# Performance work log

Measured on AMD Instinct MI355X. Metric: run time of the kernel, lower is better.

## Reference

```python
import jax, jax.numpy as jnp
import numpy as np

HEADS, KV_HEADS, HEAD_DIM = 32, 8, 64


def apply_rope(x, cos, sin):
    # x: [b,h,s,d], cos/sin: [s, d//2]; pairs are interleaved (even/odd)
    c = cos[None, None, :, :]
    s = sin[None, None, :, :]
    x1 = x[..., 0::2]
    x2 = x[..., 1::2]
    xn = x1 * c - x2 * s
    yn = x1 * s + x2 * c
    return jnp.stack([xn, yn], axis=-1).reshape(x.shape)


def setup_inputs() -> dict:
    key = jax.random.key(0)
    ks = jax.random.split(key, 7)
    b, s, h = 1, 2048, 2048
    return {
        "x": jax.random.normal(ks[0], (b, s, h), jnp.float32),
        "cos": jax.random.normal(ks[1], (s, HEAD_DIM // 2), jnp.float32),
        "sin": jax.random.normal(ks[2], (s, HEAD_DIM // 2), jnp.float32),
        "Wq": jax.random.normal(ks[3], (h, HEADS * HEAD_DIM), jnp.float32) * 0.02,
        "Wk": jax.random.normal(ks[4], (h, KV_HEADS * HEAD_DIM), jnp.float32) * 0.02,
        "Wv": jax.random.normal(ks[5], (h, KV_HEADS * HEAD_DIM), jnp.float32) * 0.02,
        "Wo": jax.random.normal(ks[6], (HEADS * HEAD_DIM, h), jnp.float32) * 0.02,
    }


def reference(x, cos, sin, Wq, Wk, Wv, Wo):
    b, seq, hidden = x.shape
    Q = x @ Wq  # [b,s,H*d]
    K = x @ Wk  # [b,s,Kh*d]
    V = x @ Wv
    q = Q.reshape(b, seq, HEADS, HEAD_DIM).transpose(0, 2, 1, 3)      # b h s d
    k = K.reshape(b, seq, KV_HEADS, HEAD_DIM).transpose(0, 2, 1, 3)   # b k s d
    v = V.reshape(b, seq, KV_HEADS, HEAD_DIM).transpose(0, 2, 1, 3)
    r = HEADS // KV_HEADS
    # einops 'b k s d -> b (r k) s d': tile kv-head block r times
    k = jnp.tile(k, (1, r, 1, 1))
    v = jnp.tile(v, (1, r, 1, 1))
    q = apply_rope(q, cos, sin)
    k = apply_rope(k, cos, sin)
    scale = 1.0 / jnp.sqrt(jnp.float32(HEAD_DIM))
    qk = jnp.einsum('bhqd,bhkd->bhqk', q, k) * scale
    mask = jnp.triu(jnp.full((seq, seq), -jnp.inf, qk.dtype), k=1)
    attn = jax.nn.softmax(qk + mask, axis=-1)
    av = jnp.einsum('bhqk,bhkd->bhqd', attn, v)
    av = av.transpose(0, 2, 1, 3).reshape(b, seq, HEADS * HEAD_DIM)
    return av @ Wo
```

## Files before the change

### kernel.cpp

```cpp
#include <hip/hip_runtime.h>

typedef unsigned short u16;
typedef __attribute__((ext_vector_type(4))) float f32x4;
typedef __attribute__((ext_vector_type(16))) float f32x16;
typedef __attribute__((ext_vector_type(8))) __bf16 bf16x8;
typedef __attribute__((ext_vector_type(2))) __bf16 bf16x2;

#define HEADS 32
#define KV_HEADS 8
#define HD 64
#define SEQ 2048
#define HID 2048
#define NQK 3072
#define QSCALE (0.125f * 1.4426950408889634f)
#define OCH 2097152u

#define AS1 __attribute__((address_space(1)))
#define AS3 __attribute__((address_space(3)))

__device__ __forceinline__ u16 f2bf(float f) {
  unsigned u = __float_as_uint(f);
  u += 0x7FFFu + ((u >> 16) & 1u);
  return (u16)(u >> 16);
}

__device__ __forceinline__ unsigned pk2(float a, float b) {
  union { bf16x2 h; unsigned u; } c;
  c.h[0] = (__bf16)a; c.h[1] = (__bf16)b;
  return c.u;
}

__device__ __forceinline__ float bflo(unsigned u) {
  return __uint_as_float(u << 16);
}
__device__ __forceinline__ float bfhi(unsigned u) {
  return __uint_as_float(u & 0xFFFF0000u);
}

__device__ __forceinline__ void load16_to_lds(const void* g, void* l) {
  __builtin_amdgcn_global_load_lds((AS1 void*)(void*)g, (AS3 void*)l, 16, 0, 0);
}

__global__ __launch_bounds__(256) void k_prep(const float* __restrict__ x,
                                              const float* __restrict__ Wq,
                                              const float* __restrict__ Wk,
                                              const float* __restrict__ Wv,
                                              const float* __restrict__ Wo,
                                              u16* __restrict__ xb,
                                              u16* __restrict__ Wqkv,
                                              u16* __restrict__ WoT) {
  __shared__ float tile[32][33];
  int bid = blockIdx.x;
  if (bid < 4096) {
    int i = bid * 256 + threadIdx.x;
    float4 v = ((const float4*)x)[i];
    ushort4 o;
    o.x = f2bf(v.x); o.y = f2bf(v.y); o.z = f2bf(v.z); o.w = f2bf(v.w);
    ((ushort4*)xb)[i] = o;
    return;
  }
  const float* in; u16* out; int ldi, cx, cy;
  if (bid < 8192) {
    int b = bid - 4096;
    in = Wq; out = Wqkv; ldi = 2048; cx = b & 63; cy = b >> 6;
  } else if (bid < 9216) {
    int b = bid - 8192;
    in = Wk; out = Wqkv + (size_t)2048 * 2048; ldi = 512; cx = b & 15; cy = b >> 4;
  } else if (bid < 10240) {
    int b = bid - 9216;
    in = Wv; out = Wqkv + (size_t)2560 * 2048; ldi = 512; cx = b & 15; cy = b >> 4;
  } else {
    int b = bid - 10240;
    in = Wo; out = WoT; ldi = 2048; cx = b & 63; cy = b >> 6;
  }
  const int ldo = 2048;
  int c0 = cx * 32, r0 = cy * 32;
  int col = threadIdx.x & 31, rw = threadIdx.x >> 5;
#pragma unroll
  for (int i = 0; i < 4; i++)
    tile[rw + i * 8][col] = in[(size_t)(r0 + rw + i * 8) * ldi + c0 + col];
  __syncthreads();
#pragma unroll
  for (int i = 0; i < 4; i++)
    out[(size_t)(c0 + rw + i * 8) * ldo + r0 + col] = f2bf(tile[col][rw + i * 8]);
}

__device__ __forceinline__ void stage8(const u16* Ap, const u16* Bp, u16* AsX,
                                       u16* BsX, int tid, int K, int koff) {
#pragma unroll
  for (int i = 0; i < 4; i++) {
    load16_to_lds(Ap + (size_t)(i * 32) * K + koff, AsX + (i * 256 + tid) * 8);
    load16_to_lds(Bp + (size_t)(i * 32) * K + koff, BsX + (i * 256 + tid) * 8);
  }
}

__device__ __forceinline__ void frag16(const u16* Asb, const u16* Bsb,
                                       const int aoff[4][2], const int boff[4][2],
                                       f32x4 acc[4][4]) {
#pragma unroll
  for (int kk = 0; kk < 2; kk++) {
    bf16x8 a[4], b[4];
#pragma unroll
    for (int i = 0; i < 4; i++)
      a[i] = *(const bf16x8*)((const char*)Asb + aoff[i][kk]);
#pragma unroll
    for (int j = 0; j < 4; j++)
      b[j] = *(const bf16x8*)((const char*)Bsb + boff[j][kk]);
#pragma unroll
    for (int i = 0; i < 4; i++)
#pragma unroll
      for (int j = 0; j < 4; j++)
        acc[i][j] = __builtin_amdgcn_mfma_f32_16x16x32_bf16(a[i], b[j], acc[i][j], 0, 0, 0);
  }
}

#define TILE_STEP(AsX, BsX, tnext)                              \
  do {                                                          \
    asm volatile("s_waitcnt vmcnt(8)" ::: "memory");            \
    __builtin_amdgcn_sched_barrier(0);                          \
    __builtin_amdgcn_s_barrier();                               \
    frag16(AsX, BsX, aoff, boff, acc);                          \
    __builtin_amdgcn_sched_barrier(0);                          \
    __builtin_amdgcn_s_barrier();                               \
    stage8(Ap, Bp, AsX, BsX, tid, K, (tnext) * 64);             \
    __builtin_amdgcn_sched_barrier(0);                          \
  } while (0)

#define TILE_TAIL(AsX, BsX, n)                                  \
  do {                                                          \
    asm volatile("s_waitcnt vmcnt(" #n ")" ::: "memory");       \
    __builtin_amdgcn_sched_barrier(0);                          \
    __builtin_amdgcn_s_barrier();                               \
    frag16(AsX, BsX, aoff, boff, acc);                          \
  } while (0)

__global__ __launch_bounds__(256) void k_gemm(const u16* __restrict__ A,
                                              const u16* __restrict__ Bt,
                                              float* __restrict__ C,
                                              int M, int N, int K) {
  __shared__ u16 smem[32768];
  u16* As0 = smem;          u16* As1 = smem + 8192;
  u16* Bs0 = smem + 16384;  u16* Bs1 = smem + 24576;
  int tid = threadIdx.x;
  int m0 = blockIdx.x * 128, n0 = blockIdx.y * 128;
  int l = tid & 63, w = tid >> 6;
  int lr = l & 15, lg = l >> 4;
  int wr = (w >> 1) * 64, wc = (w & 1) * 64;
  f32x4 acc[4][4] = {};
  int r8 = tid >> 3;
  int sx = (tid & 7) ^ (r8 & 7);
  const u16* Ap = A + (size_t)(m0 + r8) * K + sx * 8;
  const u16* Bp = Bt + (size_t)(n0 + r8) * K + sx * 8;
  int aoff[4][2], boff[4][2];
#pragma unroll
  for (int i = 0; i < 4; i++) {
    int ra = wr + i * 16 + lr;
    int rb = wc + i * 16 + lr;
#pragma unroll
    for (int kk = 0; kk < 2; kk++) {
      aoff[i][kk] = ra * 128 + (((lg + kk * 4) ^ (ra & 7)) << 4);
      boff[i][kk] = rb * 128 + (((lg + kk * 4) ^ (rb & 7)) << 4);
    }
  }
  stage8(Ap, Bp, As0, Bs0, tid, K, 0);
  stage8(Ap, Bp, As1, Bs1, tid, K, 64);
#pragma unroll 1
  for (int t = 0; t < 30; t += 2) {
    TILE_STEP(As0, Bs0, t + 2);
    TILE_STEP(As1, Bs1, t + 3);
  }
  TILE_TAIL(As0, Bs0, 8);
  TILE_TAIL(As1, Bs1, 0);

#pragma unroll
  for (int i = 0; i < 4; i++)
#pragma unroll
    for (int j = 0; j < 4; j++)
#pragma unroll
      for (int r = 0; r < 4; r++)
        C[(size_t)(m0 + wr + i * 16 + lg * 4 + r) * N + n0 + wc + j * 16 + lr] =
            acc[i][j][r];
}

__device__ __forceinline__ void stageQ(const u16* Ap, const u16* Bp, u16* S,
                                       int tid, int koff) {
#pragma unroll
  for (int i = 0; i < 2; i++)
    load16_to_lds(Ap + (size_t)(i * 32) * HID + koff, S + (i * 256 + tid) * 8);
#pragma unroll
  for (int i = 0; i < 6; i++)
    load16_to_lds(Bp + (size_t)(i * 32) * HID + koff, S + 4096 + (i * 256 + tid) * 8);
}

__device__ __forceinline__ void frag26(const u16* Sb, const int aoff[2][2],
                                       const int boff[6][2], f32x4 acc[2][6]) {
#pragma unroll
  for (int kk = 0; kk < 2; kk++) {
    bf16x8 a[2], b[6];
#pragma unroll
    for (int i = 0; i < 2; i++)
      a[i] = *(const bf16x8*)((const char*)Sb + aoff[i][kk]);
#pragma unroll
    for (int j = 0; j < 6; j++)
      b[j] = *(const bf16x8*)((const char*)Sb + 8192 + boff[j][kk]);
    __builtin_amdgcn_s_setprio(1);
#pragma unroll
    for (int i = 0; i < 2; i++)
#pragma unroll
      for (int j = 0; j < 6; j++)
        acc[i][j] = __builtin_amdgcn_mfma_f32_16x16x32_bf16(a[i], b[j], acc[i][j], 0, 0, 0);
    __builtin_amdgcn_s_setprio(0);
  }
}

#define QK_STEP(Sc, tnext)                                      \
  do {                                                          \
    asm volatile("s_waitcnt vmcnt(8)" ::: "memory");            \
    __builtin_amdgcn_sched_barrier(0);                          \
    __builtin_amdgcn_s_barrier();                               \
    frag26(Sc, aoff, boff, acc);                                \
    __builtin_amdgcn_sched_barrier(0);                          \
    __builtin_amdgcn_s_barrier();                               \
    stageQ(Ap, Bp, Sc, tid, (tnext) * 64);                      \
    __builtin_amdgcn_sched_barrier(0);                          \
  } while (0)

#define QK_TAIL(Sc, n)                                          \
  do {                                                          \
    asm volatile("s_waitcnt vmcnt(" #n ")" ::: "memory");       \
    __builtin_amdgcn_sched_barrier(0);                          \
    __builtin_amdgcn_s_barrier();                               \
    frag26(Sc, aoff, boff, acc);                                \
  } while (0)

__global__ __launch_bounds__(256) void k_gemm_qkv(const u16* __restrict__ A,
                                                  const u16* __restrict__ Bt,
                                                  const float* __restrict__ cosp,
                                                  const float* __restrict__ sinp,
                                                  u16* __restrict__ qbuf,
                                                  u16* __restrict__ kbuf,
                                                  u16* __restrict__ vtb) {
  __shared__ u16 smem[32768];
  u16* S0 = smem;
  u16* S1 = smem + 16384;
  u16* Ts = smem;
  int tid = threadIdx.x;
  int bid = blockIdx.x;
  int wg = (bid & 7) * 64 + (bid >> 3);
  int m0 = (wg & 31) * 64, n0 = (wg >> 5) * 192;
  int l = tid & 63, w = tid >> 6;
  int lr = l & 15, lg = l >> 4;
  int wr = (w >> 1) * 32, wc = (w & 1) * 96;
  f32x4 acc[2][6] = {};
  int r8 = tid >> 3;
  int sx = (tid & 7) ^ (r8 & 7);
  const u16* Ap = A + (size_t)(m0 + r8) * HID + sx * 8;
  const u16* Bp = Bt + (size_t)(n0 + r8) * HID + sx * 8;
  int aoff[2][2], boff[6][2];
#pragma unroll
  for (int i = 0; i < 2; i++) {
    int ra = wr + i * 16 + lr;
#pragma unroll
    for (int kk = 0; kk < 2; kk++)
      aoff[i][kk] = ra * 128 + (((lg + kk * 4) ^ (ra & 7)) << 4);
  }
#pragma unroll
  for (int j = 0; j < 6; j++) {
    int rb = wc + j * 16 + lr;
#pragma unroll
    for (int kk = 0; kk < 2; kk++)
      boff[j][kk] = rb * 128 + (((lg + kk * 4) ^ (rb & 7)) << 4);
  }

  stageQ(Ap, Bp, S0, tid, 0);
  stageQ(Ap, Bp, S1, tid, 64);
#pragma unroll 1
  for (int t = 0; t < 30; t += 2) {
    QK_STEP(S0, t + 2);
    QK_STEP(S1, t + 3);
  }
  QK_TAIL(S0, 8);
  QK_TAIL(S1, 0);

  int odd = lr & 1;
#pragma unroll
  for (int j = 0; j < 6; j++) {
    int colf = n0 + wc + j * 16;
    if (colf < 2560) {
      bool isQ = colf < 2048;
      float scale = isQ ? QSCALE : 1.0f;
      u16* base = isQ ? qbuf + (size_t)(colf >> 6) * SEQ * HD
                      : kbuf + (size_t)((colf - 2048) >> 6) * SEQ * HD;
      int ch = colf & 63;
      int ii = (ch >> 1) + (lr >> 1);
#pragma unroll
      for (int i = 0; i < 2; i++)
#pragma unroll
        for (int r = 0; r < 4; r++) {
          float v = acc[i][j][r];
          float vp = __shfl_xor(v, 1, 64);
          int sr = m0 + wr + i * 16 + lg * 4 + r;
          float cs = cosp[sr * 32 + ii], sn = sinp[sr * 32 + ii];
          float x1 = odd ? vp : v, x2 = odd ? v : vp;
          float o = odd ? (x1 * sn + x2 * cs) : (x1 * cs - x2 * sn);
          base[(size_t)sr * HD + ch + lr] = f2bf(o * scale);
        }
    }
  }
  if (n0 + 192 > 2560) {
    __syncthreads();
#pragma unroll
    for (int j = 0; j < 6; j++) {
      int colf = n0 + wc + j * 16;
      if (colf >= 2560) {
#pragma unroll
        for (int i = 0; i < 2; i++)
#pragma unroll
          for (int r = 0; r < 4; r++) {
            int cB = wc + j * 16 + lr, rB = wr + i * 16 + lg * 4 + r;
            *(u16*)((char*)Ts + cB * 128 + ((rB * 2) ^ ((cB & 7) << 4))) =
                f2bf(acc[i][j][r]);
          }
      }
    }
    __syncthreads();
    int half = tid & 1;
#pragma unroll
    for (int p = 0; p < 2; p++) {
      int c = p * 128 + (tid >> 1);
      if (c < 192 && n0 + c >= 2560) {
        int col = n0 + c;
        int kvh = (col - 2560) >> 6, d = col & 63;
        u16* dst = vtb + (size_t)kvh * HD * SEQ + (size_t)d * SEQ + m0 + half * 32;
        const char* src = (const char*)Ts + c * 128;
        int cs7 = (c & 7) << 4;
#pragma unroll
        for (int q = 0; q < 4; q++)
          *(uint4*)(dst + q * 8) = *(const uint4*)(src + ((half * 64 + q * 16) ^ cs7));
      }
    }
  }
}

__global__ __launch_bounds__(256) void k_flash2(const u16* __restrict__ qb,
                                                const u16* __restrict__ kb,
                                                const u16* __restrict__ vt,
                                                unsigned* __restrict__ Opart,
                                                float2* __restrict__ ml) {
  __shared__ u16 Ks[2][64 * 64];
  __shared__ u16 Vs[2][64 * 64];
  int bid = blockIdx.x;
  int c = bid & 1;
  int b5 = bid >> 1;
  int h = b5 & 31;
  int qi = b5 >> 5;
  int qblk = (SEQ / 128) - 1 - qi;
  int kvh = h & 7;
  int tid = threadIdx.x, w = tid >> 6, l = tid & 63;
  int lq = l & 31, hi = l >> 5;
  const u16* qh = qb + (size_t)h * SEQ * HD;
  const u16* kh = kb + (size_t)kvh * SEQ * HD;
  const u16* vh = vt + (size_t)kvh * HD * SEQ;
  int wq0 = qblk * 128 + w * 32;
  int qg = wq0 + lq;

  bf16x8 qf[4];
#pragma unroll
  for (int ds = 0; ds < 4; ds++)
    qf[ds] = *(const bf16x8*)(qh + (size_t)qg * HD + ds * 16 + hi * 8);

  f32x16 acc[2] = {};
  float m_r = -__builtin_inff(), l_r = 0.f;

  int srow = tid >> 2, c4 = tid & 3, swz = (srow & 7) << 4;
  int sd0 = srow * 128 + ((c4 * 32) ^ swz);
  int sd1 = srow * 128 + ((c4 * 32 + 16) ^ swz);
  const int kt0 = c * (qblk + 1), kt1 = kt0 + qblk + 1;

  {
    const u16* ksrc = kh + (size_t)(kt0 * 64 + srow) * HD + c4 * 16;
    const u16* vsrc = vh + (size_t)srow * SEQ + kt0 * 64 + c4 * 16;
    uint4 a0 = *(const uint4*)(ksrc), a1 = *(const uint4*)(ksrc + 8);
    uint4 b0 = *(const uint4*)(vsrc), b1 = *(const uint4*)(vsrc + 8);
    *(uint4*)((char*)Ks[0] + sd0) = a0; *(uint4*)((char*)Ks[0] + sd1) = a1;
    *(uint4*)((char*)Vs[0] + sd0) = b0; *(uint4*)((char*)Vs[0] + sd1) = b1;
  }
  __syncthreads();

  uint4 kr0, kr1, vr0, vr1;
  int lswz = (lq & 7) << 4;
  for (int kt = kt0; kt < kt1; kt++) {
    int b = (kt - kt0) & 1;
    if (kt + 1 < kt1) {
      const u16* ksrc = kh + (size_t)((kt + 1) * 64 + srow) * HD + c4 * 16;
      const u16* vsrc = vh + (size_t)srow * SEQ + (kt + 1) * 64 + c4 * 16;
      kr0 = *(const uint4*)(ksrc); kr1 = *(const uint4*)(ksrc + 8);
      vr0 = *(const uint4*)(vsrc); vr1 = *(const uint4*)(vsrc + 8);
    }

    if (kt * 64 <= wq0 + 31) {
      f32x16 sT[2] = {};
      const char* kbase = (const char*)Ks[b];
      __builtin_amdgcn_s_setprio(1);
#pragma unroll
      for (int t = 0; t < 2; t++) {
#pragma unroll
        for (int ds = 0; ds < 4; ds++) {
          bf16x8 kf = *(const bf16x8*)(kbase + (t * 32 + lq) * 128 +
                                       ((ds * 32 + hi * 16) ^ lswz));
          sT[t] = __builtin_amdgcn_mfma_f32_32x32x16_bf16(kf, qf[ds], sT[t], 0, 0, 0);
        }
      }
      __builtin_amdgcn_s_setprio(0);

      if (kt * 64 + 63 > wq0) {
#pragma unroll
        for (int t = 0; t < 2; t++)
#pragma unroll
          for (int r = 0; r < 16; r++) {
            int kg = kt * 64 + t * 32 + (r & 3) + 8 * (r >> 2) + 4 * hi;
            if (kg > qg) sT[t][r] = -__builtin_inff();
          }
      }

      float pmax = sT[0][0];
#pragma unroll
      for (int r = 1; r < 16; r++) pmax = fmaxf(pmax, sT[0][r]);
#pragma unroll
      for (int r = 0; r < 16; r++) pmax = fmaxf(pmax, sT[1][r]);
      pmax = fmaxf(pmax, __shfl_xor(pmax, 32, 64));

      if (!__all(pmax <= m_r + 8.f)) {
        float mn = fmaxf(m_r, pmax);
        float scl = __builtin_amdgcn_exp2f(m_r - mn);
        l_r *= scl;
        acc[0] *= scl;
        acc[1] *= scl;
        m_r = mn;
      }

      float ss = 0.f;
#pragma unroll
      for (int t = 0; t < 2; t++)
#pragma unroll
        for (int r = 0; r < 16; r++) {
          float p = __builtin_amdgcn_exp2f(sT[t][r] - m_r);
          sT[t][r] = p;
          ss += p;
        }
      ss += __shfl_xor(ss, 32, 64);
      l_r += ss;

      const char* vbase = (const char*)Vs[b];
#pragma unroll
      for (int t = 0; t < 2; t++) {
        unsigned cp[4][2];
#pragma unroll
        for (int m = 0; m < 4; m++) {
          cp[m][0] = pk2(sT[t][4 * m + 0], sT[t][4 * m + 1]);
          cp[m][1] = pk2(sT[t][4 * m + 2], sT[t][4 * m + 3]);
        }
#pragma unroll
        for (int kl = 0; kl < 2; kl++) {
          unsigned s0 = hi ? cp[2 * kl][0] : cp[2 * kl + 1][0];
          unsigned s1 = hi ? cp[2 * kl][1] : cp[2 * kl + 1][1];
          unsigned r0 = (unsigned)__shfl_xor((int)s0, 32, 64);
          unsigned r1 = (unsigned)__shfl_xor((int)s1, 32, 64);
          union { unsigned u[4]; bf16x8 v; } pa;
          pa.u[0] = hi ? r0 : cp[2 * kl][0];
          pa.u[1] = hi ? r1 : cp[2 * kl][1];
          pa.u[2] = hi ? cp[2 * kl + 1][0] : r0;
          pa.u[3] = hi ? cp[2 * kl + 1][1] : r1;
          int ks = t * 2 + kl;
          __builtin_amdgcn_s_setprio(1);
#pragma unroll
          for (int dt = 0; dt < 2; dt++) {
            bf16x8 vb = *(const bf16x8*)(vbase + (dt * 32 + lq) * 128 +
                                         ((ks * 32 + hi * 16) ^ lswz));
            acc[dt] = __builtin_amdgcn_mfma_f32_32x32x16_bf16(vb, pa.v, acc[dt], 0, 0, 0);
          }
          __builtin_amdgcn_s_setprio(0);
        }
      }
    }

    if (kt + 1 < kt1) {
      *(uint4*)((char*)Ks[b ^ 1] + sd0) = kr0;
      *(uint4*)((char*)Ks[b ^ 1] + sd1) = kr1;
      *(uint4*)((char*)Vs[b ^ 1] + sd0) = vr0;
      *(uint4*)((char*)Vs[b ^ 1] + sd1) = vr1;
    }
    __syncthreads();
  }

  unsigned* op = Opart + (size_t)c * OCH + ((size_t)(b5 * 4 + w) * 16) * 64;
#pragma unroll
  for (int dt = 0; dt < 2; dt++)
#pragma unroll
    for (int j = 0; j < 8; j++)
      op[(dt * 8 + j) * 64 + l] = pk2(acc[dt][2 * j], acc[dt][2 * j + 1]);
  if (!hi)
    ml[c * (HEADS * SEQ) + h * SEQ + wq0 + lq] = make_float2(m_r, l_r);
}

__global__ __launch_bounds__(256) void k_merge(const unsigned* __restrict__ Opart,
                                               const float2* __restrict__ ml,
                                               u16* __restrict__ av) {
  __shared__ u16 Ts[8192];
  int bid = blockIdx.x;
  int h = bid & 31, qblk = bid >> 5;
  int b5 = ((SEQ / 128 - 1 - qblk) << 5) | h;
  int tid = threadIdx.x, w = tid >> 6, l = tid & 63;
  int lq = l & 31, hi = l >> 5;
  int wq0 = qblk * 128 + w * 32;

  float2 ml0 = ml[h * SEQ + wq0 + lq];
  float2 ml1 = ml[HEADS * SEQ + h * SEQ + wq0 + lq];
  float m = fmaxf(ml0.x, ml1.x);
  float f0 = __builtin_amdgcn_exp2f(ml0.x - m);
  float f1 = __builtin_amdgcn_exp2f(ml1.x - m);
  float inv = 1.0f / (ml0.y * f0 + ml1.y * f1);

  const unsigned* op0 = Opart + ((size_t)(b5 * 4 + w) * 16) * 64;
  const unsigned* op1 = op0 + OCH;
  f32x16 acc[2];
#pragma unroll
  for (int dt = 0; dt < 2; dt++)
#pragma unroll
    for (int j = 0; j < 8; j++) {
      unsigned a0 = op0[(dt * 8 + j) * 64 + l];
      unsigned a1 = op1[(dt * 8 + j) * 64 + l];
      acc[dt][2 * j] = bflo(a0) * f0 + bflo(a1) * f1;
      acc[dt][2 * j + 1] = bfhi(a0) * f0 + bfhi(a1) * f1;
    }

  int lswz = (lq & 7) << 4;
  char* wbase = (char*)Ts + w * 4096;
#pragma unroll
  for (int dt = 0; dt < 2; dt++)
#pragma unroll
    for (int m4 = 0; m4 < 4; m4++) {
      int r0 = 4 * m4;
      uint2 pr;
      pr.x = pk2(acc[dt][r0 + 0] * inv, acc[dt][r0 + 1] * inv);
      pr.y = pk2(acc[dt][r0 + 2] * inv, acc[dt][r0 + 3] * inv);
      int byte = lq * 128 + ((dt * 64 + m4 * 16 + hi * 8) ^ lswz);
      *(uint2*)(wbase + byte) = pr;
    }
  __syncthreads();
  int q2 = l >> 1, cH = l & 1;
  int qswz = (q2 & 7) << 4;
#pragma unroll
  for (int i = 0; i < 4; i++) {
    uint4 d = *(const uint4*)(wbase + q2 * 128 + ((cH * 64 + i * 16) ^ qswz));
    *(uint4*)(av + (size_t)(wq0 + q2) * HID + h * HD + cH * 32 + i * 8) = d;
  }
}

extern "C" void kernel_launch(void* const* d_in, const int* in_sizes, int n_in,
                              void* d_out, int out_size, void* d_ws, size_t ws_size,
                              hipStream_t stream) {
  (void)in_sizes; (void)n_in; (void)out_size; (void)ws_size;
  const float* x = (const float*)d_in[0];
  const float* cosp = (const float*)d_in[1];
  const float* sinp = (const float*)d_in[2];
  const float* Wq = (const float*)d_in[3];
  const float* Wk = (const float*)d_in[4];
  const float* Wv = (const float*)d_in[5];
  const float* Wo = (const float*)d_in[6];
  float* out = (float*)d_out;
  char* ws = (char*)d_ws;

  u16* xb = (u16*)(ws);
  float2* mlb = (float2*)(ws);
  u16* Wqkv = (u16*)(ws + ((size_t)8 << 20));
  u16* WoT = (u16*)(ws + ((size_t)20 << 20));
  u16* qbuf = (u16*)(ws + ((size_t)28 << 20));
  u16* kbuf = (u16*)(ws + ((size_t)36 << 20));
  u16* vtb = (u16*)(ws + ((size_t)38 << 20));
  u16* av = (u16*)(ws + ((size_t)40 << 20));
  unsigned* Opart = (unsigned*)(ws + ((size_t)48 << 20));

  k_prep<<<14336, 256, 0, stream>>>(x, Wq, Wk, Wv, Wo, xb, Wqkv, WoT);
  k_gemm_qkv<<<512, 256, 0, stream>>>(xb, Wqkv, cosp, sinp, qbuf, kbuf, vtb);
  k_flash2<<<(SEQ / 128) * HEADS * 2, 256, 0, stream>>>(qbuf, kbuf, vtb, Opart, mlb);
  k_merge<<<(SEQ / 128) * HEADS, 256, 0, stream>>>(Opart, mlb, av);
  k_gemm<<<dim3(SEQ / 128, HID / 128), 256, 0, stream>>>(av, WoT, out, SEQ, HID, HID);
}
```

Measured before the change: 116.0 us.

## Fuse split-KV merge into flash kernel via last-arriver atomic counter

Removes the separate k_merge launch. Each flash block fences its partial output, then bumps a per-(qblock,head) counter with an agent-scope atomic, and the second block to arrive does the merge and writes av. The counters live in the output buffer, are zeroed by block 0 of the QKV GEMM, and are later overwritten by the final GEMM. This saves one kernel launch and its tail, at the cost of an atomic and an imbalanced epilogue on the last-arriving blocks. It reuses Ks smem as scratch, which assumes the loop's final __syncthreads has completed.

```diff
diff --git a/kernel.cpp b/kernel.cpp
--- a/kernel.cpp
+++ b/kernel.cpp
@@ -239,12 +239,17 @@
                                                   const float* __restrict__ sinp,
                                                   u16* __restrict__ qbuf,
                                                   u16* __restrict__ kbuf,
-                                                  u16* __restrict__ vtb) {
+                                                  u16* __restrict__ vtb,
+                                                  unsigned* __restrict__ flags) {
   __shared__ u16 smem[32768];
   u16* S0 = smem;
   u16* S1 = smem + 16384;
   u16* Ts = smem;
   int tid = threadIdx.x;
+  if (blockIdx.x == 0) {
+    flags[tid] = 0;
+    flags[tid + 256] = 0;
+  }
   int bid = blockIdx.x;
   int wg = (bid & 7) * 64 + (bid >> 3);
   int m0 = (wg & 31) * 64, n0 = (wg >> 5) * 192;
@@ -346,9 +351,12 @@
                                                 const u16* __restrict__ kb,
                                                 const u16* __restrict__ vt,
                                                 unsigned* __restrict__ Opart,
-                                                float2* __restrict__ ml) {
+                                                float2* __restrict__ ml,
+                                                u16* __restrict__ av,
+                                                unsigned* __restrict__ flags) {
   __shared__ u16 Ks[2][64 * 64];
   __shared__ u16 Vs[2][64 * 64];
+  __shared__ unsigned winner;
   int bid = blockIdx.x;
   int c = bid & 1;
   int b5 = bid >> 1;
@@ -501,59 +509,54 @@
       op[(dt * 8 + j) * 64 + l] = pk2(acc[dt][2 * j], acc[dt][2 * j + 1]);
   if (!hi)
     ml[c * (HEADS * SEQ) + h * SEQ + wq0 + lq] = make_float2(m_r, l_r);
-}
-
-__global__ __launch_bounds__(256) void k_merge(const unsigned* __restrict__ Opart,
-                                               const float2* __restrict__ ml,
-                                               u16* __restrict__ av) {
-  __shared__ u16 Ts[8192];
-  int bid = blockIdx.x;
-  int h = bid & 31, qblk = bid >> 5;
-  int b5 = ((SEQ / 128 - 1 - qblk) << 5) | h;
-  int tid = threadIdx.x, w = tid >> 6, l = tid & 63;
-  int lq = l & 31, hi = l >> 5;
-  int wq0 = qblk * 128 + w * 32;
-
-  float2 ml0 = ml[h * SEQ + wq0 + lq];
-  float2 ml1 = ml[HEADS * SEQ + h * SEQ + wq0 + lq];
-  float m = fmaxf(ml0.x, ml1.x);
-  float f0 = __builtin_amdgcn_exp2f(ml0.x - m);
-  float f1 = __builtin_amdgcn_exp2f(ml1.x - m);
-  float inv = 1.0f / (ml0.y * f0 + ml1.y * f1);
-
-  const unsigned* op0 = Opart + ((size_t)(b5 * 4 + w) * 16) * 64;
-  const unsigned* op1 = op0 + OCH;
-  f32x16 acc[2];
-#pragma unroll
-  for (int dt = 0; dt < 2; dt++)
-#pragma unroll
-    for (int j = 0; j < 8; j++) {
-      unsigned a0 = op0[(dt * 8 + j) * 64 + l];
-      unsigned a1 = op1[(dt * 8 + j) * 64 + l];
-      acc[dt][2 * j] = bflo(a0) * f0 + bflo(a1) * f1;
-      acc[dt][2 * j + 1] = bfhi(a0) * f0 + bfhi(a1) * f1;
-    }
-
-  int lswz = (lq & 7) << 4;
-  char* wbase = (char*)Ts + w * 4096;
-#pragma unroll
-  for (int dt = 0; dt < 2; dt++)
-#pragma unroll
-    for (int m4 = 0; m4 < 4; m4++) {
-      int r0 = 4 * m4;
-      uint2 pr;
-      pr.x = pk2(acc[dt][r0 + 0] * inv, acc[dt][r0 + 1] * inv);
-      pr.y = pk2(acc[dt][r0 + 2] * inv, acc[dt][r0 + 3] * inv);
-      int byte = lq * 128 + ((dt * 64 + m4 * 16 + hi * 8) ^ lswz);
-      *(uint2*)(wbase + byte) = pr;
-    }
+
+  __threadfence();
   __syncthreads();
-  int q2 = l >> 1, cH = l & 1;
-  int qswz = (q2 & 7) << 4;
-#pragma unroll
-  for (int i = 0; i < 4; i++) {
-    uint4 d = *(const uint4*)(wbase + q2 * 128 + ((cH * 64 + i * 16) ^ qswz));
-    *(uint4*)(av + (size_t)(wq0 + q2) * HID + h * HD + cH * 32 + i * 8) = d;
+  if (tid == 0)
+    winner = __hip_atomic_fetch_add(&flags[b5], 1u, __ATOMIC_ACQ_REL,
+                                    __HIP_MEMORY_SCOPE_AGENT);
+  __syncthreads();
+  if (winner == 1) {
+    float2 ml0 = ml[h * SEQ + wq0 + lq];
+    float2 ml1 = ml[HEADS * SEQ + h * SEQ + wq0 + lq];
+    float mm = fmaxf(ml0.x, ml1.x);
+    float f0 = __builtin_amdgcn_exp2f(ml0.x - mm);
+    float f1 = __builtin_amdgcn_exp2f(ml1.x - mm);
+    float inv = 1.0f / (ml0.y * f0 + ml1.y * f1);
+
+    const unsigned* mop0 = Opart + ((size_t)(b5 * 4 + w) * 16) * 64;
+    const unsigned* mop1 = mop0 + OCH;
+    f32x16 macc[2];
+#pragma unroll
+    for (int dt = 0; dt < 2; dt++)
+#pragma unroll
+      for (int j = 0; j < 8; j++) {
+        unsigned a0 = mop0[(dt * 8 + j) * 64 + l];
+        unsigned a1 = mop1[(dt * 8 + j) * 64 + l];
+        macc[dt][2 * j] = bflo(a0) * f0 + bflo(a1) * f1;
+        macc[dt][2 * j + 1] = bfhi(a0) * f0 + bfhi(a1) * f1;
+      }
+
+    char* wbase = (char*)Ks[0] + w * 4096;
+#pragma unroll
+    for (int dt = 0; dt < 2; dt++)
+#pragma unroll
+      for (int m4 = 0; m4 < 4; m4++) {
+        int r0 = 4 * m4;
+        uint2 pr;
+        pr.x = pk2(macc[dt][r0 + 0] * inv, macc[dt][r0 + 1] * inv);
+        pr.y = pk2(macc[dt][r0 + 2] * inv, macc[dt][r0 + 3] * inv);
+        int byte = lq * 128 + ((dt * 64 + m4 * 16 + hi * 8) ^ lswz);
+        *(uint2*)(wbase + byte) = pr;
+      }
+    __syncthreads();
+    int q2 = l >> 1, cH = l & 1;
+    int qswz = (q2 & 7) << 4;
+#pragma unroll
+    for (int i = 0; i < 4; i++) {
+      uint4 d = *(const uint4*)(wbase + q2 * 128 + ((cH * 64 + i * 16) ^ qswz));
+      *(uint4*)(av + (size_t)(wq0 + q2) * HID + h * HD + cH * 32 + i * 8) = d;
+    }
   }
 }
 
@@ -580,10 +583,11 @@
   u16* vtb = (u16*)(ws + ((size_t)38 << 20));
   u16* av = (u16*)(ws + ((size_t)40 << 20));
   unsigned* Opart = (unsigned*)(ws + ((size_t)48 << 20));
+  unsigned* flags = (unsigned*)out;
 
   k_prep<<<14336, 256, 0, stream>>>(x, Wq, Wk, Wv, Wo, xb, Wqkv, WoT);
-  k_gemm_qkv<<<512, 256, 0, stream>>>(xb, Wqkv, cosp, sinp, qbuf, kbuf, vtb);
-  k_flash2<<<(SEQ / 128) * HEADS * 2, 256, 0, stream>>>(qbuf, kbuf, vtb, Opart, mlb);
-  k_merge<<<(SEQ / 128) * HEADS, 256, 0, stream>>>(Opart, mlb, av);
+  k_gemm_qkv<<<512, 256, 0, stream>>>(xb, Wqkv, cosp, sinp, qbuf, kbuf, vtb, flags);
+  k_flash2<<<(SEQ / 128) * HEADS * 2, 256, 0, stream>>>(qbuf, kbuf, vtb, Opart,
+                                                        mlb, av, flags);
   k_gemm<<<dim3(SEQ / 128, HID / 128), 256, 0, stream>>>(av, WoT, out, SEQ, HID, HID);
 }
```

Measured after the change: 245.6 us. +111.8%, slower.
